# Performance work log

Hardware: AMD Instinct MI355X
Metric: run time of the kernel (lower is better)

The kernel has to match this reference:

```python
import jax, jax.numpy as jnp
import numpy as np

H = 64   # hid_dim (hard-coded in Attn_LSTM)
C = 8    # enc_in / out_dim
L = 96   # enc_seq_len = interval*lag = max_length
T = 24   # pre_len = window*horizon
B = 4096


def _p(key, shape, scale=0.1):
    return (jax.random.normal(key, shape, dtype=jnp.float32) * scale)


def setup_inputs() -> dict:
    key = jax.random.key(0)
    ks = jax.random.split(key, 20)
    inp = {
        'x_enc': jax.random.normal(ks[0], (B, L, C), dtype=jnp.float32),
        'x_mark_enc': jax.random.normal(ks[1], (B, L, 4), dtype=jnp.float32),
        'x_dec': jax.random.normal(ks[2], (B, T, C), dtype=jnp.float32),
        'x_mark_dec': jax.random.normal(ks[3], (B, T, 4), dtype=jnp.float32),
        # encoder LSTM (1 layer, input C -> hid H), pytorch gate order i,f,g,o
        'enc_Wih': _p(ks[4], (4 * H, C)), 'enc_Whh': _p(ks[5], (4 * H, H)),
        'enc_bih': _p(ks[6], (4 * H,)), 'enc_bhh': _p(ks[7], (4 * H,)),
        # decoder
        'emb_W': _p(ks[8], (H, C)), 'emb_b': _p(ks[9], (H,)),
        'attn_W': _p(ks[10], (L, 2 * H)), 'attn_b': _p(ks[11], (L,)),
        'comb_W': _p(ks[12], (H, 2 * H)), 'comb_b': _p(ks[13], (H,)),
        'dec_Wih': _p(ks[14], (4 * H, H)), 'dec_Whh': _p(ks[15], (4 * H, H)),
        'dec_bih': _p(ks[16], (4 * H,)), 'dec_bhh': _p(ks[17], (4 * H,)),
        'out_W': _p(ks[18], (C, H)), 'out_b': _p(ks[19], (C,)),
    }
    return inp


def _lstm_cell(x, h, c, Wih, Whh, bih, bhh):
    g = x @ Wih.T + h @ Whh.T + (bih + bhh)
    i, f, gg, o = jnp.split(g, 4, axis=-1)
    i, f, o = jax.nn.sigmoid(i), jax.nn.sigmoid(f), jax.nn.sigmoid(o)
    c_new = f * c + i * jnp.tanh(gg)
    h_new = o * jnp.tanh(c_new)
    return h_new, c_new


def _forward(x_enc, enc_Wih, enc_Whh, enc_bih, enc_bhh,
             emb_W, emb_b, attn_W, attn_b, comb_W, comb_b,
             dec_Wih, dec_Whh, dec_bih, dec_bhh, out_W, out_b):
    seq_last = x_enc[:, -1:, :]               # [B,1,C]
    x = x_enc - seq_last                      # normalized

    # ---- encoder: 1-layer LSTM over L steps ----
    h0 = jnp.zeros((x.shape[0], H), dtype=x.dtype)
    c0 = jnp.zeros_like(h0)

    def enc_step(carry, xt):
        h, c = carry
        h, c = _lstm_cell(xt, h, c, enc_Wih, enc_Whh, enc_bih, enc_bhh)
        return (h, c), h

    (h_enc, c_enc), enc_out = jax.lax.scan(enc_step, (h0, c0),
                                           jnp.swapaxes(x, 0, 1))
    enc_out = jnp.swapaxes(enc_out, 0, 1)     # [B,L,H]

    # ---- attention decoder: T sequential steps ----
    dec_in0 = x[:, -1, :]                     # last (normalized) input, [B,C]

    def dec_step(carry, _):
        inp, h, c = carry
        emb = jax.nn.relu(inp @ emb_W.T + emb_b)                       # [B,H]
        aw = jax.nn.softmax(jnp.concatenate([emb, h], -1) @ attn_W.T + attn_b)  # [B,L]
        ctx = jnp.einsum('bl,blh->bh', aw, enc_out)                    # [B,H]
        comb = jnp.concatenate([emb, ctx], -1) @ comb_W.T + comb_b     # [B,H]
        h, c = _lstm_cell(comb, h, c, dec_Wih, dec_Whh, dec_bih, dec_bhh)
        pred = h @ out_W.T + out_b                                     # [B,C]
        # original code feeds prediction.detach() back in
        return (jax.lax.stop_gradient(pred), h, c), (pred, aw)

    _, (preds, aws) = jax.lax.scan(dec_step, (dec_in0, h_enc, c_enc),
                                   None, length=T)
    pre_y = jnp.swapaxes(preds, 0, 1) + seq_last   # [B,T,C]
    return pre_y


def reference(x_enc, x_mark_enc, x_dec, x_mark_dec,
              enc_Wih, enc_Whh, enc_bih, enc_bhh,
              emb_W, emb_b, attn_W, attn_b, comb_W, comb_b,
              dec_Wih, dec_Whh, dec_bih, dec_bhh, out_W, out_b):
    # x_mark_enc, x_dec, x_mark_dec are accepted but unused (as in original)
    return _forward(x_enc, enc_Wih, enc_Whh, enc_bih, enc_bhh,
                    emb_W, emb_b, attn_W, attn_b, comb_W, comb_b,
                    dec_Wih, dec_Whh, dec_bih, dec_bhh, out_W, out_b)
```

## Files before the change

### kernel.cpp

```cpp
#include <hip/hip_runtime.h>

#define LL 96
#define TT 24
#define HH 64
#define CC 8
#define GG 256
#define BT 8
#define NB 512

typedef unsigned short u16t;
typedef unsigned int   u32t;
typedef __attribute__((ext_vector_type(8))) short bf16x8;
typedef __attribute__((ext_vector_type(4))) float f32x4;

__device__ __forceinline__ float b2f(u16t u){ union{u32t i; float f;} v; v.i=((u32t)u)<<16; return v.f; }
__device__ __forceinline__ u16t f2b(float f){ union{float f; u32t i;} v; v.f=f; u32t l=(v.i>>16)&1u; v.i+=0x7fffu+l; return (u16t)(v.i>>16); }
__device__ __forceinline__ float rcpf(float x){ return __builtin_amdgcn_rcpf(x); }
__device__ __forceinline__ float sigm(float x){ return rcpf(1.f + __expf(-x)); }
__device__ __forceinline__ float tanh2(float x){ return 1.f - 2.f*rcpf(__expf(2.f*x) + 1.f); }
__device__ __forceinline__ u32t pk2(float a, float b){ return (u32t)f2b(a) | ((u32t)f2b(b)<<16); }
__device__ __forceinline__ bf16x8 u2b8(uint4 u){ union{uint4 a; bf16x8 b;} v; v.a=u; return v.b; }
__device__ __forceinline__ int aaddr(int k, int m){ return (((k>>5)*4 + ((k>>3)&3))*16 + m)*8 + (k&7); }

__device__ __forceinline__ void bar_lds(){
    asm volatile("s_waitcnt lgkmcnt(0)" ::: "memory");
    __builtin_amdgcn_s_barrier();
    asm volatile("" ::: "memory");
    __builtin_amdgcn_sched_barrier(0);
}

template<bool F32> __device__ __forceinline__ float ldf(const void* p, size_t i){
    if constexpr (F32) return ((const float*)p)[i];
    else               return b2f(((const u16t*)p)[i]);
}
template<bool F32> __device__ __forceinline__ uint4 ld8p(const void* p, size_t i){
    if constexpr (F32){
        const float* f = (const float*)p + i;
        uint4 r; r.x = pk2(f[0],f[1]); r.y = pk2(f[2],f[3]);
                 r.z = pk2(f[4],f[5]); r.w = pk2(f[6],f[7]);
        return r;
    } else return *(const uint4*)((const u16t*)p + i);
}
template<bool F32> __device__ __forceinline__ void stf(void* p, size_t i, float v){
    if constexpr (F32) ((float*)p)[i] = v;
    else               ((u16t*)p)[i] = f2b(v);
}
template<bool F32> __device__ __forceinline__ float ldW_enc(const void* wih, const void* whh, int r, int k){
    if (k < CC)      return ldf<F32>(wih, (size_t)r*CC + k);
    else if (k < 72) return ldf<F32>(whh, (size_t)r*HH + (k-CC));
    else             return 0.f;
}

__device__ __forceinline__ bool inputs_are_f32(const void* bih){
    const u16t* p = (const u16t*)bih;
    int cnt = 0;
    #pragma unroll
    for (int i = 0; i < 64; ++i){
        u32t e = ((u32t)p[i] >> 7) & 0xFFu;
        cnt += (e >= 128u) ? 1 : 0;
    }
    return cnt > 0;
}

template<bool F32>
__global__ __launch_bounds__(256,4) void enc4_g(
    const void* __restrict__ x_enc,
    const void* __restrict__ eWih, const void* __restrict__ eWhh,
    const void* __restrict__ ebih, const void* __restrict__ ebhh,
    u16t* __restrict__ eoG, float* __restrict__ cG)
{
    if (inputs_are_f32(ebih) != F32) return;

    __shared__ __align__(16) short Abuf2[2][1536];

    const int tid = threadIdx.x;
    const int b0  = blockIdx.x * 4;
    const int col = tid & 15, quad = (tid >> 4) & 3, wv = tid >> 6;

    bf16x8 Bf[4][3];
    float  biasg[4];
    #pragma unroll
    for (int g = 0; g < 4; ++g){
        int r = g*64 + wv*16 + col;
        biasg[g] = ldf<F32>(ebih, r) + ldf<F32>(ebhh, r);
        #pragma unroll
        for (int kb = 0; kb < 3; ++kb){
            bf16x8 v;
            #pragma unroll
            for (int x = 0; x < 8; ++x){
                int k = kb*32 + quad*8 + x;
                v[x] = (short)f2b(ldW_enc<F32>(eWih, eWhh, r, k));
            }
            Bf[g][kb] = v;
        }
    }
    for (int n = tid; n < 2*1536; n += 256) ((short*)Abuf2)[n] = 0;
    float sl = 0.f; size_t xbase = 0;
    if (tid < 32){ int b = tid >> 3, i = tid & 7;
        xbase = (size_t)(b0+b)*(LL*CC) + i;
        sl = ldf<F32>(x_enc, xbase + (size_t)(LL-1)*CC);
    }
    __syncthreads();
    if (tid < 32){ short v = (short)f2b(ldf<F32>(x_enc, xbase) - sl);
        Abuf2[0][tid] = v; Abuf2[0][tid+32] = v; Abuf2[0][tid+64] = v; Abuf2[0][tid+96] = v; }
    float xr = (tid < 32) ? ldf<F32>(x_enc, xbase + CC) : 0.f;

    const int jmy = wv*16 + col;
    const int hwbase = aaddr(8 + jmy, 0);
    const u32t ebase = ((u32t)(b0 + quad)*4u + (u32t)(jmy>>4))*1536u + (u32t)((jmy&15)*8);

    float creg = 0.f;
    u32t  pkv  = 0;

    #pragma unroll 2
    for (int t = 0; t < LL; ++t){
        bar_lds();
        const bf16x8* AbR = (const bf16x8*)Abuf2[t & 1];
        short*        AbW = Abuf2[(t + 1) & 1];
        bf16x8 a0 = AbR[(0*4 + quad)*16 + col];
        bf16x8 a1 = AbR[(1*4 + quad)*16 + col];
        bf16x8 a2 = AbR[(2*4 + quad)*16 + col];
        f32x4 acc[4];
        #pragma unroll
        for (int g = 0; g < 4; ++g){
            f32x4 a; a[0]=biasg[g]; a[1]=biasg[g]; a[2]=biasg[g]; a[3]=biasg[g];
            a = __builtin_amdgcn_mfma_f32_16x16x32_bf16(a0, Bf[g][0], a, 0,0,0);
            a = __builtin_amdgcn_mfma_f32_16x16x32_bf16(a1, Bf[g][1], a, 0,0,0);
            a = __builtin_amdgcn_mfma_f32_16x16x32_bf16(a2, Bf[g][2], a, 0,0,0);
            acc[g] = a;
        }
        float c = sigm(acc[1][quad])*creg + sigm(acc[0][quad])*tanh2(acc[2][quad]);
        float h = sigm(acc[3][quad])*tanh2(c);
        creg = c;
        u16t hb = f2b(h);
        if ((t & 1) == 0) pkv = hb;
        else {
            pkv |= ((u32t)hb) << 16;
            *(u32t*)&eoG[ebase + (u32t)((t>>5)*512 + ((t>>3)&3)*128 + (t&7) - 1)] = pkv;
        }
        AbW[hwbase + quad*8]      = (short)hb;
        AbW[hwbase + quad*8+32]   = (short)hb;
        AbW[hwbase + quad*8+64]   = (short)hb;
        AbW[hwbase + quad*8+96]   = (short)hb;
        if (tid < 32 && t < LL-1){
            short v = (short)f2b(xr - sl);
            AbW[tid] = v; AbW[tid+32] = v; AbW[tid+64] = v; AbW[tid+96] = v;
            int tn = (t+2 < LL) ? t+2 : LL-1;
            xr = ldf<F32>(x_enc, xbase + (size_t)tn*CC);
        }
    }
    cG[(size_t)(b0 + quad)*HH + jmy] = creg;
}

template<bool F32>
__global__ __launch_bounds__(256,2) void dec8_g(
    const void* __restrict__ x_enc,
    const void* __restrict__ embW, const void* __restrict__ embb,
    const void* __restrict__ attnW, const void* __restrict__ attnb,
    const void* __restrict__ combW, const void* __restrict__ combb,
    const void* __restrict__ dWih, const void* __restrict__ dWhh,
    const void* __restrict__ dbih, const void* __restrict__ dbhh,
    const void* __restrict__ outW, const void* __restrict__ outb,
    void* __restrict__ outp, const u16t* __restrict__ eoG,
    const float* __restrict__ cG)
{
    if (inputs_are_f32(dbih) != F32) return;

    __shared__ __align__(16) float slp[CC*10];
    __shared__ __align__(16) char  uni[18880];
    __shared__ __align__(16) u16t BaL[6*4*4*16*8];
    __shared__ __align__(16) u16t emBL[64*8];
    __shared__ __align__(16) u16t oWL[8*64];

    const int tid = threadIdx.x;
    const int b0  = blockIdx.x * BT;
    const int col = tid & 15, quad = (tid >> 4) & 3, wv = tid >> 6;
    const int r0  = (quad >> 1) * 2;
    const int jmy = wv*16 + col;

    if (tid < BT*CC){ int b = tid >> 3, i = tid & 7;
        slp[i*10 + b] = ldf<F32>(x_enc, (size_t)(b0+b)*(LL*CC) + (size_t)(LL-1)*CC + i); }

    bf16x8 Bd[4][4];
    #pragma unroll
    for (int g = 0; g < 4; ++g){
        int r = g*64 + wv*16 + col;
        Bd[g][0] = u2b8(ld8p<F32>(dWih, (size_t)r*HH + quad*8));
        Bd[g][1] = u2b8(ld8p<F32>(dWih, (size_t)r*HH + 32 + quad*8));
        Bd[g][2] = u2b8(ld8p<F32>(dWhh, (size_t)r*HH + quad*8));
        Bd[g][3] = u2b8(ld8p<F32>(dWhh, (size_t)r*HH + 32 + quad*8));
    }
    bf16x8 Bc[4];
    #pragma unroll
    for (int kb = 0; kb < 4; ++kb)
        Bc[kb] = u2b8(ld8p<F32>(combW, (size_t)(wv*16+col)*128 + kb*32 + quad*8));
    bf16x8 zz = {0,0,0,0,0,0,0,0};

    for (int idx = tid; idx < 1536; idx += 256){
        int lt_ = idx >> 8, kb_ = (idx >> 6) & 3, q_ = (idx >> 4) & 3, c_ = idx & 15;
        int row = lt_*16 + c_;
        u16t tmp[8];
        #pragma unroll
        for (int x = 0; x < 8; ++x)
            tmp[x] = f2b(ldf<F32>(attnW, (size_t)row*128 + kb_*32 + q_*8 + x));
        *(uint4*)&BaL[(size_t)idx*8] = *(uint4*)tmp;
    }
    if (tid < 64){
        u16t tmp[8];
        #pragma unroll
        for (int c = 0; c < 8; ++c) tmp[c] = f2b(ldf<F32>(embW, (size_t)tid*CC + c));
        *(uint4*)&emBL[tid*8] = *(uint4*)tmp;
    }
    for (int n = tid; n < 512; n += 256) oWL[n] = f2b(ldf<F32>(outW, n));

    float* decB  = (float*)(uni + 0);
    float* attnB = (float*)(uni + 1024);
    float* embB  = (float*)(uni + 1408);
    float* combB = (float*)(uni + 1664);
    float* outB  = (float*)(uni + 1920);
    float* Lg    = (float*)(uni + 1952);
    u16t*  awB   = (u16t*)(uni + 5024);
    u16t*  Ae    = (u16t*)(uni + 6560);
    u16t*  Ah0   = (u16t*)(uni + 8608);
    u16t*  Ah1   = (u16t*)(uni + 10656);
    u16t*  Actx  = (u16t*)(uni + 12704);
    u16t*  Acmb  = (u16t*)(uni + 14752);
    u16t*  Apred = (u16t*)(uni + 16800);

    float creg[2];
    #pragma unroll
    for (int rr = 0; rr < 2; ++rr){
        int b = (quad*4 + r0 + rr) & 7;
        u16t hv = eoG[(((size_t)(b0+b)*4 + (size_t)(jmy>>4))*3 + 2)*512 + 3*128 + (jmy&15)*8 + 7];
        Ah0[aaddr(jmy, b)]   = hv;
        Ah0[aaddr(jmy, b+8)] = hv;
        creg[rr] = cG[(size_t)(b0+b)*HH + jmy];
    }
    decB[tid] = ldf<F32>(dbih, tid) + ldf<F32>(dbhh, tid);
    if (tid < LL) attnB[tid] = ldf<F32>(attnb, tid);
    if (tid < HH) embB[tid]  = ldf<F32>(embb, tid);
    if (tid < HH) combB[tid] = ldf<F32>(combb, tid);
    if (tid < CC) outB[tid]  = ldf<F32>(outb, tid);
    for (int n = tid; n < 1024; n += 256) Apred[n] = 0;
    __syncthreads();

    const u16t* ebp = eoG + (size_t)(b0 + wv*2) * 6144;
    uint4 eF0[12], eF1[12];
    #pragma unroll
    for (int f = 0; f < 12; ++f) eF0[f] = *(const uint4*)(ebp + f*512 + quad*128 + col*8);
    #pragma unroll
    for (int f = 0; f < 12; ++f) eF1[f] = *(const uint4*)(ebp + 6144 + f*512 + quad*128 + col*8);

    const int lgS = tid & 31, bS = tid >> 5;
    const bf16x8* AeV   = (const bf16x8*)Ae;
    const bf16x8* ActxV = (const bf16x8*)Actx;
    const bf16x8* AcmbV = (const bf16x8*)Acmb;
    const bf16x8* ApV   = (const bf16x8*)Apred;

    for (int t = 0; t < TT; ++t){
        u16t* AhR = (t & 1) ? Ah1 : Ah0;
        u16t* AhW = (t & 1) ? Ah0 : Ah1;
        const bf16x8* AhV = (const bf16x8*)AhR;

        {
            bf16x8 ap = ApV[quad*16 + col];
            bf16x8 eBf = zz;
            if (quad == 0) eBf = *(const bf16x8*)&emBL[(wv*16+col)*8];
            float eb = embB[wv*16 + col];
            f32x4 a; a[0]=eb; a[1]=eb; a[2]=eb; a[3]=eb;
            a = __builtin_amdgcn_mfma_f32_16x16x32_bf16(ap, eBf, a, 0,0,0);
            #pragma unroll
            for (int r = 0; r < 4; ++r)
                Ae[aaddr(wv*16+col, quad*4 + r)] = f2b(fmaxf(a[r], 0.f));
        }
        bar_lds();

        {
            bf16x8 ae0 = AeV[(0*4+quad)*16 + col], ae1 = AeV[(1*4+quad)*16 + col];
            bf16x8 ah0 = AhV[(0*4+quad)*16 + col], ah1 = AhV[(1*4+quad)*16 + col];
            const int ns = (wv < 2) ? 2 : 1;
            for (int s = 0; s < ns; ++s){
                int lt = (s == 0) ? wv : 4+wv;
                const u16t* bp = &BaL[lt*2048 + quad*128 + col*8];
                float bz = attnB[lt*16 + col];
                f32x4 a; a[0]=bz; a[1]=bz; a[2]=bz; a[3]=bz;
                a = __builtin_amdgcn_mfma_f32_16x16x32_bf16(ae0, *(const bf16x8*)&bp[0],    a, 0,0,0);
                a = __builtin_amdgcn_mfma_f32_16x16x32_bf16(ae1, *(const bf16x8*)&bp[512],  a, 0,0,0);
                a = __builtin_amdgcn_mfma_f32_16x16x32_bf16(ah0, *(const bf16x8*)&bp[1024], a, 0,0,0);
                a = __builtin_amdgcn_mfma_f32_16x16x32_bf16(ah1, *(const bf16x8*)&bp[1536], a, 0,0,0);
                if (quad < 2)
                    *(float4*)&Lg[(lt*16+col)*8 + quad*4] = make_float4(a[0],a[1],a[2],a[3]);
            }
        }
        bar_lds();

        {
            int l = lgS*3;
            float ev0 = Lg[l*8 + bS], ev1 = Lg[(l+1)*8 + bS], ev2 = Lg[(l+2)*8 + bS];
            float mx = fmaxf(ev0, fmaxf(ev1, ev2));
            #pragma unroll
            for (int m = 16; m >= 1; m >>= 1) mx = fmaxf(mx, __shfl_xor(mx, m, 32));
            float e0 = __expf(ev0 - mx), e1 = __expf(ev1 - mx), e2 = __expf(ev2 - mx);
            float sm = e0 + e1 + e2;
            #pragma unroll
            for (int m = 16; m >= 1; m >>= 1) sm += __shfl_xor(sm, m, 32);
            float inv = rcpf(sm);
            awB[bS*96 + l]     = f2b(e0*inv);
            awB[bS*96 + l + 1] = f2b(e1*inv);
            awB[bS*96 + l + 2] = f2b(e2*inv);
        }
        {
            const u16t* ap0 = awB + (wv*2)*96;
            bf16x8 f0 = *(const bf16x8*)(ap0 + quad*8);
            bf16x8 f1 = *(const bf16x8*)(ap0 + 32 + quad*8);
            bf16x8 f2 = *(const bf16x8*)(ap0 + 64 + quad*8);
            #pragma unroll
            for (int nt = 0; nt < 4; ++nt){
                f32x4 a; a[0]=0.f; a[1]=0.f; a[2]=0.f; a[3]=0.f;
                a = __builtin_amdgcn_mfma_f32_16x16x32_bf16(f0, u2b8(eF0[nt*3+0]), a, 0,0,0);
                a = __builtin_amdgcn_mfma_f32_16x16x32_bf16(f1, u2b8(eF0[nt*3+1]), a, 0,0,0);
                a = __builtin_amdgcn_mfma_f32_16x16x32_bf16(f2, u2b8(eF0[nt*3+2]), a, 0,0,0);
                if (quad == 0){
                    u16t v = f2b(a[0]);
                    Actx[aaddr(nt*16+col, wv*2)]   = v;
                    Actx[aaddr(nt*16+col, wv*2+8)] = v;
                }
            }
            const u16t* ap1 = awB + (wv*2+1)*96;
            bf16x8 g0 = *(const bf16x8*)(ap1 + quad*8);
            bf16x8 g1 = *(const bf16x8*)(ap1 + 32 + quad*8);
            bf16x8 g2 = *(const bf16x8*)(ap1 + 64 + quad*8);
            #pragma unroll
            for (int nt = 0; nt < 4; ++nt){
                f32x4 a; a[0]=0.f; a[1]=0.f; a[2]=0.f; a[3]=0.f;
                a = __builtin_amdgcn_mfma_f32_16x16x32_bf16(g0, u2b8(eF1[nt*3+0]), a, 0,0,0);
                a = __builtin_amdgcn_mfma_f32_16x16x32_bf16(g1, u2b8(eF1[nt*3+1]), a, 0,0,0);
                a = __builtin_amdgcn_mfma_f32_16x16x32_bf16(g2, u2b8(eF1[nt*3+2]), a, 0,0,0);
                if (quad == 0){
                    u16t v = f2b(a[0]);
                    Actx[aaddr(nt*16+col, wv*2+1)] = v;
                    Actx[aaddr(nt*16+col, wv*2+9)] = v;
                }
            }
        }
        bar_lds();

        {
            bf16x8 ae0 = AeV[(0*4+quad)*16 + col],   ae1 = AeV[(1*4+quad)*16 + col];
            bf16x8 ax0 = ActxV[(0*4+quad)*16 + col], ax1 = ActxV[(1*4+quad)*16 + col];
            float bz = combB[wv*16 + col];
            f32x4 a; a[0]=bz; a[1]=bz; a[2]=bz; a[3]=bz;
            a = __builtin_amdgcn_mfma_f32_16x16x32_bf16(ae0, Bc[0], a, 0,0,0);
            a = __builtin_amdgcn_mfma_f32_16x16x32_bf16(ae1, Bc[1], a, 0,0,0);
            a = __builtin_amdgcn_mfma_f32_16x16x32_bf16(ax0, Bc[2], a, 0,0,0);
            a = __builtin_amdgcn_mfma_f32_16x16x32_bf16(ax1, Bc[3], a, 0,0,0);
            #pragma unroll
            for (int r = 0; r < 4; ++r)
                Acmb[aaddr(wv*16+col, quad*4 + r)] = f2b(a[r]);
        }
        bar_lds();

        {
            bf16x8 ac0 = AcmbV[(0*4+quad)*16 + col], ac1 = AcmbV[(1*4+quad)*16 + col];
            bf16x8 ah0 = AhV[(0*4+quad)*16 + col],   ah1 = AhV[(1*4+quad)*16 + col];
            f32x4 g4[4];
            #pragma unroll
            for (int g = 0; g < 4; ++g){
                float bz = decB[g*64 + wv*16 + col];
                f32x4 a; a[0]=bz; a[1]=bz; a[2]=bz; a[3]=bz;
                a = __builtin_amdgcn_mfma_f32_16x16x32_bf16(ac0, Bd[g][0], a, 0,0,0);
                a = __builtin_amdgcn_mfma_f32_16x16x32_bf16(ac1, Bd[g][1], a, 0,0,0);
                a = __builtin_amdgcn_mfma_f32_16x16x32_bf16(ah0, Bd[g][2], a, 0,0,0);
                a = __builtin_amdgcn_mfma_f32_16x16x32_bf16(ah1, Bd[g][3], a, 0,0,0);
                g4[g] = a;
            }
            #pragma unroll
            for (int rr = 0; rr < 2; ++rr){
                int r = r0 + rr;
                int b = (quad*4 + r) & 7;
                float c = sigm(g4[1][r])*creg[rr] + sigm(g4[0][r])*tanh2(g4[2][r]);
                float h = sigm(g4[3][r])*tanh2(c);
                creg[rr] = c;
                u16t hv = f2b(h);
                AhW[aaddr(jmy, b)]   = hv;
                AhW[aaddr(jmy, b+8)] = hv;
            }
        }
        bar_lds();

        if (wv == 0){
            const bf16x8* AhWV = (const bf16x8*)AhW;
            bf16x8 xh0 = AhWV[(0*4+quad)*16 + col];
            bf16x8 xh1 = AhWV[(1*4+quad)*16 + col];
            bf16x8 oBf0 = zz, oBf1 = zz;
            if (col < CC){
                oBf0 = *(const bf16x8*)&oWL[col*64 + quad*8];
                oBf1 = *(const bf16x8*)&oWL[col*64 + 32 + quad*8];
            }
            float ob = outB[col & 7];
            f32x4 a; a[0]=ob; a[1]=ob; a[2]=ob; a[3]=ob;
            a = __builtin_amdgcn_mfma_f32_16x16x32_bf16(xh0, oBf0, a, 0,0,0);
            a = __builtin_amdgcn_mfma_f32_16x16x32_bf16(xh1, oBf1, a, 0,0,0);
            if (col < CC){
                #pragma unroll
                for (int r = 0; r < 4; ++r){
                    int m = quad*4 + r, b = m & 7;
                    float p = a[r];
                    Apred[aaddr(col, m)] = f2b(p);
                    if (m < 8)
                        stf<F32>(outp, ((size_t)(b0+b)*TT + t)*CC + col, p + slp[col*10 + b]);
                }
            }
        }
        bar_lds();
    }
}

template<bool F32>
__global__ __launch_bounds__(256,2) void fused_g(
    const void* __restrict__ x_enc,
    const void* __restrict__ eWih, const void* __restrict__ eWhh,
    const void* __restrict__ ebih, const void* __restrict__ ebhh,
    const void* __restrict__ embW, const void* __restrict__ embb,
    const void* __restrict__ attnW, const void* __restrict__ attnb,
    const void* __restrict__ combW, const void* __restrict__ combb,
    const void* __restrict__ dWih, const void* __restrict__ dWhh,
    const void* __restrict__ dbih, const void* __restrict__ dbhh,
    const void* __restrict__ outW, const void* __restrict__ outb,
    void* __restrict__ outp, u16t* __restrict__ eoG)
{
    if (inputs_are_f32(ebih) != F32) return;

    __shared__ __align__(16) float slp[CC*10];
    __shared__ __align__(16) short Abuf2[2][1536];
    __shared__ __align__(16) char  uni[18880];

    const int tid = threadIdx.x;
    const int b0  = blockIdx.x * BT;
    const int col = tid & 15, quad = (tid >> 4) & 3, wv = tid >> 6;
    const int r0  = (quad >> 1) * 2;

    bf16x8 Bf[4][3];
    float  biasg[4];
    #pragma unroll
    for (int g = 0; g < 4; ++g){
        int r = g*64 + wv*16 + col;
        biasg[g] = ldf<F32>(ebih, r) + ldf<F32>(ebhh, r);
        #pragma unroll
        for (int kb = 0; kb < 3; ++kb){
            bf16x8 v;
            #pragma unroll
            for (int x = 0; x < 8; ++x){
                int k = kb*32 + quad*8 + x;
                v[x] = (short)f2b(ldW_enc<F32>(eWih, eWhh, r, k));
            }
            Bf[g][kb] = v;
        }
    }
    for (int n = tid; n < 2*1536; n += 256) ((short*)Abuf2)[n] = 0;
    float sl = 0.f; size_t xbase = 0;
    if (tid < BT*CC){ int b = tid >> 3, i = tid & 7;
        xbase = (size_t)(b0+b)*(LL*CC) + i;
        sl = ldf<F32>(x_enc, xbase + (size_t)(LL-1)*CC);
        slp[i*10 + b] = sl; }
    __syncthreads();
    if (tid < BT*CC){ short v = (short)f2b(ldf<F32>(x_enc, xbase) - sl);
        Abuf2[0][tid] = v; Abuf2[0][tid + 64] = v; }
    float xr = (tid < BT*CC) ? ldf<F32>(x_enc, xbase + CC) : 0.f;

    const int jmy = wv*16 + col;
    const int kh  = 8 + jmy;
    const int hwbase = aaddr(kh, 0);

    u32t ebase[2];
    #pragma unroll
    for (int rr = 0; rr < 2; ++rr){
        u32t bg = (u32t)(b0 + ((quad*4 + r0 + rr) & 7));
        ebase[rr] = (bg*4u + (u32t)(jmy>>4))*1536u + (u32t)((jmy&15)*8);
    }

    float creg[2] = {0.f,0.f};
    u16t  hb16[2] = {0,0};

    for (int t = 0; t < LL; ++t){
        __syncthreads();
        const bf16x8* AbR = (const bf16x8*)Abuf2[t & 1];
        short*        AbW = Abuf2[(t + 1) & 1];
        bf16x8 a0 = AbR[(0*4 + quad)*16 + col];
        bf16x8 a1 = AbR[(1*4 + quad)*16 + col];
        bf16x8 a2 = AbR[(2*4 + quad)*16 + col];
        f32x4 acc[4];
        #pragma unroll
        for (int g = 0; g < 4; ++g){
            f32x4 a; a[0]=biasg[g]; a[1]=biasg[g]; a[2]=biasg[g]; a[3]=biasg[g];
            a = __builtin_amdgcn_mfma_f32_16x16x32_bf16(a0, Bf[g][0], a, 0,0,0);
            a = __builtin_amdgcn_mfma_f32_16x16x32_bf16(a1, Bf[g][1], a, 0,0,0);
            a = __builtin_amdgcn_mfma_f32_16x16x32_bf16(a2, Bf[g][2], a, 0,0,0);
            acc[g] = a;
        }
        int off = (t>>5)*512 + ((t>>3)&3)*128 + (t&7);
        #pragma unroll
        for (int rr = 0; rr < 2; ++rr){
            int r = r0 + rr;
            int b = (quad*4 + r) & 7;
            float c = sigm(acc[1][r])*creg[rr] + sigm(acc[0][r])*tanh2(acc[2][r]);
            float h = sigm(acc[3][r])*tanh2(c);
            creg[rr] = c; hb16[rr] = f2b(h);
            eoG[ebase[rr] + off] = hb16[rr];
            AbW[hwbase + b*8]     = (short)hb16[rr];
            AbW[hwbase + (b+8)*8] = (short)hb16[rr];
        }
        if (tid < BT*CC && t < LL-1){
            short v = (short)f2b(xr - sl);
            AbW[tid] = v; AbW[tid + 64] = v;
            int tn = (t+2 < LL) ? t+2 : LL-1;
            xr = ldf<F32>(x_enc, xbase + (size_t)tn*CC);
        }
    }

    bf16x8 Bd[4][4];
    #pragma unroll
    for (int g = 0; g < 4; ++g){
        int r = g*64 + wv*16 + col;
        Bd[g][0] = u2b8(ld8p<F32>(dWih, (size_t)r*HH + quad*8));
        Bd[g][1] = u2b8(ld8p<F32>(dWih, (size_t)r*HH + 32 + quad*8));
        Bd[g][2] = u2b8(ld8p<F32>(dWhh, (size_t)r*HH + quad*8));
        Bd[g][3] = u2b8(ld8p<F32>(dWhh, (size_t)r*HH + 32 + quad*8));
    }
    bf16x8 Ba[2][4];
    #pragma unroll
    for (int kb = 0; kb < 4; ++kb)
        Ba[0][kb] = u2b8(ld8p<F32>(attnW, (size_t)(wv*16+col)*128 + kb*32 + quad*8));
    if (wv < 2){
        #pragma unroll
        for (int kb = 0; kb < 4; ++kb)
            Ba[1][kb] = u2b8(ld8p<F32>(attnW, (size_t)((4+wv)*16+col)*128 + kb*32 + quad*8));
    } else {
        #pragma unroll
        for (int kb = 0; kb < 4; ++kb) Ba[1][kb] = Ba[0][kb];
    }
    bf16x8 Bc[4];
    #pragma unroll
    for (int kb = 0; kb < 4; ++kb)
        Bc[kb] = u2b8(ld8p<F32>(combW, (size_t)(wv*16+col)*128 + kb*32 + quad*8));
    bf16x8 zz = {0,0,0,0,0,0,0,0};
    bf16x8 eBf = zz;
    if (quad == 0) eBf = u2b8(ld8p<F32>(embW, (size_t)(wv*16+col)*CC));
    bf16x8 oBf0 = zz, oBf1 = zz;
    if (col < CC){
        oBf0 = u2b8(ld8p<F32>(outW, (size_t)col*HH + quad*8));
        oBf1 = u2b8(ld8p<F32>(outW, (size_t)col*HH + 32 + quad*8));
    }

    float* decB  = (float*)(uni + 0);
    float* attnB = (float*)(uni + 1024);
    float* embB  = (float*)(uni + 1408);
    float* combB = (float*)(uni + 1664);
    float* outB  = (float*)(uni + 1920);
    float* Lg    = (float*)(uni + 1952);
    u16t*  awB   = (u16t*)(uni + 5024);
    u16t*  Ae    = (u16t*)(uni + 6560);
    u16t*  Ah0   = (u16t*)(uni + 8608);
    u16t*  Ah1   = (u16t*)(uni + 10656);
    u16t*  Actx  = (u16t*)(uni + 12704);
    u16t*  Acmb  = (u16t*)(uni + 14752);
    u16t*  Apred = (u16t*)(uni + 16800);

    #pragma unroll
    for (int rr = 0; rr < 2; ++rr){
        int b = (quad*4 + r0 + rr) & 7;
        Ah0[aaddr(jmy, b)]     = hb16[rr];
        Ah0[aaddr(jmy, b+8)]   = hb16[rr];
    }
    decB[tid] = ldf<F32>(dbih, tid) + ldf<F32>(dbhh, tid);
    if (tid < LL) attnB[tid] = ldf<F32>(attnb, tid);
    if (tid < HH) embB[tid]  = ldf<F32>(embb, tid);
    if (tid < HH) combB[tid] = ldf<F32>(combb, tid);
    if (tid < CC) outB[tid]  = ldf<F32>(outb, tid);
    for (int n = tid; n < 1024; n += 256) Apred[n] = 0;
    __syncthreads();

    const u16t* ebp = eoG + (size_t)(b0 + wv*2) * 6144;
    uint4 eF0[12], eF1[12];
    #pragma unroll
    for (int f = 0; f < 12; ++f) eF0[f] = *(const uint4*)(ebp + f*512 + quad*128 + col*8);
    #pragma unroll
    for (int f = 0; f < 12; ++f) eF1[f] = *(const uint4*)(ebp + 6144 + f*512 + quad*128 + col*8);

    const int lgS = tid & 31, bS = tid >> 5;
    const bf16x8* AeV   = (const bf16x8*)Ae;
    const bf16x8* ActxV = (const bf16x8*)Actx;
    const bf16x8* AcmbV = (const bf16x8*)Acmb;
    const bf16x8* ApV   = (const bf16x8*)Apred;

    for (int t = 0; t < TT; ++t){
        u16t* AhR = (t & 1) ? Ah1 : Ah0;
        u16t* AhW = (t & 1) ? Ah0 : Ah1;
        const bf16x8* AhV = (const bf16x8*)AhR;

        {
            bf16x8 ap = ApV[quad*16 + col];
            float eb = embB[wv*16 + col];
            f32x4 a; a[0]=eb; a[1]=eb; a[2]=eb; a[3]=eb;
            a = __builtin_amdgcn_mfma_f32_16x16x32_bf16(ap, eBf, a, 0,0,0);
            #pragma unroll
            for (int r = 0; r < 4; ++r)
                Ae[aaddr(wv*16+col, quad*4 + r)] = f2b(fmaxf(a[r], 0.f));
        }
        __syncthreads();

        {
            bf16x8 ae0 = AeV[(0*4+quad)*16 + col], ae1 = AeV[(1*4+quad)*16 + col];
            bf16x8 ah0 = AhV[(0*4+quad)*16 + col], ah1 = AhV[(1*4+quad)*16 + col];
            const int ns = (wv < 2) ? 2 : 1;
            for (int s = 0; s < ns; ++s){
                int lt = (s == 0) ? wv : 4+wv;
                float bz = attnB[lt*16 + col];
                f32x4 a; a[0]=bz; a[1]=bz; a[2]=bz; a[3]=bz;
                a = __builtin_amdgcn_mfma_f32_16x16x32_bf16(ae0, Ba[s][0], a, 0,0,0);
                a = __builtin_amdgcn_mfma_f32_16x16x32_bf16(ae1, Ba[s][1], a, 0,0,0);
                a = __builtin_amdgcn_mfma_f32_16x16x32_bf16(ah0, Ba[s][2], a, 0,0,0);
                a = __builtin_amdgcn_mfma_f32_16x16x32_bf16(ah1, Ba[s][3], a, 0,0,0);
                if (quad < 2)
                    *(float4*)&Lg[(lt*16+col)*8 + quad*4] = make_float4(a[0],a[1],a[2],a[3]);
            }
        }
        __syncthreads();

        {
            int l = lgS*3;
            float ev0 = Lg[l*8 + bS], ev1 = Lg[(l+1)*8 + bS], ev2 = Lg[(l+2)*8 + bS];
            float mx = fmaxf(ev0, fmaxf(ev1, ev2));
            #pragma unroll
            for (int m = 16; m >= 1; m >>= 1) mx = fmaxf(mx, __shfl_xor(mx, m, 32));
            float e0 = __expf(ev0 - mx), e1 = __expf(ev1 - mx), e2 = __expf(ev2 - mx);
            float sm = e0 + e1 + e2;
            #pragma unroll
            for (int m = 16; m >= 1; m >>= 1) sm += __shfl_xor(sm, m, 32);
            float inv = rcpf(sm);
            awB[bS*96 + l]     = f2b(e0*inv);
            awB[bS*96 + l + 1] = f2b(e1*inv);
            awB[bS*96 + l + 2] = f2b(e2*inv);
        }
        {
            const u16t* ap0 = awB + (wv*2)*96;
            bf16x8 f0 = *(const bf16x8*)(ap0 + quad*8);
            bf16x8 f1 = *(const bf16x8*)(ap0 + 32 + quad*8);
            bf16x8 f2 = *(const bf16x8*)(ap0 + 64 + quad*8);
            #pragma unroll
            for (int nt = 0; nt < 4; ++nt){
                f32x4 a; a[0]=0.f; a[1]=0.f; a[2]=0.f; a[3]=0.f;
                a = __builtin_amdgcn_mfma_f32_16x16x32_bf16(f0, u2b8(eF0[nt*3+0]), a, 0,0,0);
                a = __builtin_amdgcn_mfma_f32_16x16x32_bf16(f1, u2b8(eF0[nt*3+1]), a, 0,0,0);
                a = __builtin_amdgcn_mfma_f32_16x16x32_bf16(f2, u2b8(eF0[nt*3+2]), a, 0,0,0);
                if (quad == 0){
                    u16t v = f2b(a[0]);
                    Actx[aaddr(nt*16+col, wv*2)]   = v;
                    Actx[aaddr(nt*16+col, wv*2+8)] = v;
                }
            }
            const u16t* ap1 = awB + (wv*2+1)*96;
            bf16x8 g0 = *(const bf16x8*)(ap1 + quad*8);
            bf16x8 g1 = *(const bf16x8*)(ap1 + 32 + quad*8);
            bf16x8 g2 = *(const bf16x8*)(ap1 + 64 + quad*8);
            #pragma unroll
            for (int nt = 0; nt < 4; ++nt){
                f32x4 a; a[0]=0.f; a[1]=0.f; a[2]=0.f; a[3]=0.f;
                a = __builtin_amdgcn_mfma_f32_16x16x32_bf16(g0, u2b8(eF1[nt*3+0]), a, 0,0,0);
                a = __builtin_amdgcn_mfma_f32_16x16x32_bf16(g1, u2b8(eF1[nt*3+1]), a, 0,0,0);
                a = __builtin_amdgcn_mfma_f32_16x16x32_bf16(g2, u2b8(eF1[nt*3+2]), a, 0,0,0);
                if (quad == 0){
                    u16t v = f2b(a[0]);
                    Actx[aaddr(nt*16+col, wv*2+1)] = v;
                    Actx[aaddr(nt*16+col, wv*2+9)] = v;
                }
            }
        }
        __syncthreads();

        {
            bf16x8 ae0 = AeV[(0*4+quad)*16 + col],   ae1 = AeV[(1*4+quad)*16 + col];
            bf16x8 ax0 = ActxV[(0*4+quad)*16 + col], ax1 = ActxV[(1*4+quad)*16 + col];
            float bz = combB[wv*16 + col];
            f32x4 a; a[0]=bz; a[1]=bz; a[2]=bz; a[3]=bz;
            a = __builtin_amdgcn_mfma_f32_16x16x32_bf16(ae0, Bc[0], a, 0,0,0);
            a = __builtin_amdgcn_mfma_f32_16x16x32_bf16(ae1, Bc[1], a, 0,0,0);
            a = __builtin_amdgcn_mfma_f32_16x16x32_bf16(ax0, Bc[2], a, 0,0,0);
            a = __builtin_amdgcn_mfma_f32_16x16x32_bf16(ax1, Bc[3], a, 0,0,0);
            #pragma unroll
            for (int r = 0; r < 4; ++r)
                Acmb[aaddr(wv*16+col, quad*4 + r)] = f2b(a[r]);
        }
        __syncthreads();

        {
            bf16x8 ac0 = AcmbV[(0*4+quad)*16 + col], ac1 = AcmbV[(1*4+quad)*16 + col];
            bf16x8 ah0 = AhV[(0*4+quad)*16 + col],   ah1 = AhV[(1*4+quad)*16 + col];
            f32x4 g4[4];
            #pragma unroll
            for (int g = 0; g < 4; ++g){
                float bz = decB[g*64 + wv*16 + col];
                f32x4 a; a[0]=bz; a[1]=bz; a[2]=bz; a[3]=bz;
                a = __builtin_amdgcn_mfma_f32_16x16x32_bf16(ac0, Bd[g][0], a, 0,0,0);
                a = __builtin_amdgcn_mfma_f32_16x16x32_bf16(ac1, Bd[g][1], a, 0,0,0);
                a = __builtin_amdgcn_mfma_f32_16x16x32_bf16(ah0, Bd[g][2], a, 0,0,0);
                a = __builtin_amdgcn_mfma_f32_16x16x32_bf16(ah1, Bd[g][3], a, 0,0,0);
                g4[g] = a;
            }
            #pragma unroll
            for (int rr = 0; rr < 2; ++rr){
                int r = r0 + rr;
                int b = (quad*4 + r) & 7;
                float c = sigm(g4[1][r])*creg[rr] + sigm(g4[0][r])*tanh2(g4[2][r]);
                float h = sigm(g4[3][r])*tanh2(c);
                creg[rr] = c;
                u16t hv = f2b(h);
                AhW[aaddr(jmy, b)]   = hv;
                AhW[aaddr(jmy, b+8)] = hv;
            }
        }
        __syncthreads();

        if (wv == 0){
            const bf16x8* AhWV = (const bf16x8*)AhW;
            bf16x8 xh0 = AhWV[(0*4+quad)*16 + col];
            bf16x8 xh1 = AhWV[(1*4+quad)*16 + col];
            float ob = outB[col & 7];
            f32x4 a; a[0]=ob; a[1]=ob; a[2]=ob; a[3]=ob;
            a = __builtin_amdgcn_mfma_f32_16x16x32_bf16(xh0, oBf0, a, 0,0,0);
            a = __builtin_amdgcn_mfma_f32_16x16x32_bf16(xh1, oBf1, a, 0,0,0);
            if (col < CC){
                #pragma unroll
                for (int r = 0; r < 4; ++r){
                    int m = quad*4 + r, b = m & 7;
                    float p = a[r];
                    Apred[aaddr(col, m)] = f2b(p);
                    if (m < 8)
                        stf<F32>(outp, ((size_t)(b0+b)*TT + t)*CC + col, p + slp[col*10 + b]);
                }
            }
        }
        __syncthreads();
    }
}

extern "C" void kernel_launch(void* const* d_in, const int* in_sizes, int n_in,
                              void* d_out, int out_size, void* d_ws, size_t ws_size,
                              hipStream_t stream)
{
    (void)in_sizes; (void)n_in; (void)out_size;
    u16t* eoG = (u16t*)d_ws;
    if (ws_size >= 50331648ull + 1048576ull){
        float* cG = (float*)((char*)d_ws + 50331648ull);
        enc4_g<false><<<1024, 256, 0, stream>>>(
            d_in[0], d_in[4], d_in[5], d_in[6], d_in[7], eoG, cG);
        enc4_g<true ><<<1024, 256, 0, stream>>>(
            d_in[0], d_in[4], d_in[5], d_in[6], d_in[7], eoG, cG);
        dec8_g<false><<<NB, 256, 0, stream>>>(
            d_in[0],
            d_in[8],  d_in[9],  d_in[10], d_in[11],
            d_in[12], d_in[13], d_in[14], d_in[15],
            d_in[16], d_in[17], d_in[18], d_in[19],
            d_out, eoG, cG);
        dec8_g<true ><<<NB, 256, 0, stream>>>(
            d_in[0],
            d_in[8],  d_in[9],  d_in[10], d_in[11],
            d_in[12], d_in[13], d_in[14], d_in[15],
            d_in[16], d_in[17], d_in[18], d_in[19],
            d_out, eoG, cG);
    } else {
        fused_g<false><<<NB, 256, 0, stream>>>(
            d_in[0],
            d_in[4],  d_in[5],  d_in[6],  d_in[7],
            d_in[8],  d_in[9],  d_in[10], d_in[11],
            d_in[12], d_in[13], d_in[14], d_in[15],
            d_in[16], d_in[17], d_in[18], d_in[19],
            d_out, eoG);
        fused_g<true><<<NB, 256, 0, stream>>>(
            d_in[0],
            d_in[4],  d_in[5],  d_in[6],  d_in[7],
            d_in[8],  d_in[9],  d_in[10], d_in[11],
            d_in[12], d_in[13], d_in[14], d_in[15],
            d_in[16], d_in[17], d_in[18], d_in[19],
            d_out, eoG);
    }
}
```

Measured before the change: 279.3 us.

## Fold output projection into embedding weights and drop softmax max-subtraction

```diff
diff --git a/kernel.cpp b/kernel.cpp
--- a/kernel.cpp
+++ b/kernel.cpp
@@ -167,9 +167,9 @@
     if (inputs_are_f32(dbih) != F32) return;
 
     __shared__ __align__(16) float slp[CC*10];
-    __shared__ __align__(16) char  uni[18880];
+    __shared__ __align__(16) char  uni[16800];
     __shared__ __align__(16) u16t BaL[6*4*4*16*8];
-    __shared__ __align__(16) u16t emBL[64*8];
+    __shared__ __align__(16) u16t M1L[64*64];
     __shared__ __align__(16) u16t oWL[8*64];
 
     const int tid = threadIdx.x;
@@ -205,17 +205,26 @@
             tmp[x] = f2b(ldf<F32>(attnW, (size_t)row*128 + kb_*32 + q_*8 + x));
         *(uint4*)&BaL[(size_t)idx*8] = *(uint4*)tmp;
     }
-    if (tid < 64){
-        u16t tmp[8];
-        #pragma unroll
-        for (int c = 0; c < 8; ++c) tmp[c] = f2b(ldf<F32>(embW, (size_t)tid*CC + c));
-        *(uint4*)&emBL[tid*8] = *(uint4*)tmp;
+    for (int idx = tid; idx < 1024; idx += 256){
+        int j = idx >> 4, k0 = (idx & 15) * 4;
+        float acc4[4] = {0.f,0.f,0.f,0.f};
+        #pragma unroll
+        for (int c = 0; c < 8; ++c){
+            float e = ldf<F32>(embW, (size_t)j*CC + c);
+            #pragma unroll
+            for (int kk = 0; kk < 4; ++kk)
+                acc4[kk] += e * ldf<F32>(outW, (size_t)c*HH + k0 + kk);
+        }
+        u16t tmp[4];
+        #pragma unroll
+        for (int kk = 0; kk < 4; ++kk) tmp[kk] = f2b(acc4[kk]);
+        *(uint2*)&M1L[j*64 + k0] = *(uint2*)tmp;
     }
     for (int n = tid; n < 512; n += 256) oWL[n] = f2b(ldf<F32>(outW, n));
 
     float* decB  = (float*)(uni + 0);
     float* attnB = (float*)(uni + 1024);
-    float* embB  = (float*)(uni + 1408);
+    float* b1B   = (float*)(uni + 1408);
     float* combB = (float*)(uni + 1664);
     float* outB  = (float*)(uni + 1920);
     float* Lg    = (float*)(uni + 1952);
@@ -225,7 +234,6 @@
     u16t*  Ah1   = (u16t*)(uni + 10656);
     u16t*  Actx  = (u16t*)(uni + 12704);
     u16t*  Acmb  = (u16t*)(uni + 14752);
-    u16t*  Apred = (u16t*)(uni + 16800);
 
     float creg[2];
     #pragma unroll
@@ -238,10 +246,22 @@
     }
     decB[tid] = ldf<F32>(dbih, tid) + ldf<F32>(dbhh, tid);
     if (tid < LL) attnB[tid] = ldf<F32>(attnb, tid);
-    if (tid < HH) embB[tid]  = ldf<F32>(embb, tid);
+    if (tid < HH){
+        float s = ldf<F32>(embb, tid);
+        #pragma unroll
+        for (int c = 0; c < 8; ++c)
+            s += ldf<F32>(embW, (size_t)tid*CC + c) * ldf<F32>(outb, c);
+        b1B[tid] = s;
+    }
     if (tid < HH) combB[tid] = ldf<F32>(combb, tid);
     if (tid < CC) outB[tid]  = ldf<F32>(outb, tid);
-    for (int n = tid; n < 1024; n += 256) Apred[n] = 0;
+    {
+        float e0v = fmaxf(ldf<F32>(embb, jmy), 0.f);
+        u16t ev = f2b(e0v);
+        #pragma unroll
+        for (int r = 0; r < 4; ++r)
+            Ae[aaddr(jmy, quad*4 + r)] = ev;
+    }
     __syncthreads();
 
     const u16t* ebp = eoG + (size_t)(b0 + wv*2) * 6144;
@@ -255,25 +275,11 @@
     const bf16x8* AeV   = (const bf16x8*)Ae;
     const bf16x8* ActxV = (const bf16x8*)Actx;
     const bf16x8* AcmbV = (const bf16x8*)Acmb;
-    const bf16x8* ApV   = (const bf16x8*)Apred;
 
     for (int t = 0; t < TT; ++t){
         u16t* AhR = (t & 1) ? Ah1 : Ah0;
         u16t* AhW = (t & 1) ? Ah0 : Ah1;
         const bf16x8* AhV = (const bf16x8*)AhR;
-
-        {
-            bf16x8 ap = ApV[quad*16 + col];
-            bf16x8 eBf = zz;
-            if (quad == 0) eBf = *(const bf16x8*)&emBL[(wv*16+col)*8];
-            float eb = embB[wv*16 + col];
-            f32x4 a; a[0]=eb; a[1]=eb; a[2]=eb; a[3]=eb;
-            a = __builtin_amdgcn_mfma_f32_16x16x32_bf16(ap, eBf, a, 0,0,0);
-            #pragma unroll
-            for (int r = 0; r < 4; ++r)
-                Ae[aaddr(wv*16+col, quad*4 + r)] = f2b(fmaxf(a[r], 0.f));
-        }
-        bar_lds();
 
         {
             bf16x8 ae0 = AeV[(0*4+quad)*16 + col], ae1 = AeV[(1*4+quad)*16 + col];
@@ -296,11 +302,7 @@
 
         {
             int l = lgS*3;
-            float ev0 = Lg[l*8 + bS], ev1 = Lg[(l+1)*8 + bS], ev2 = Lg[(l+2)*8 + bS];
-            float mx = fmaxf(ev0, fmaxf(ev1, ev2));
-            #pragma unroll
-            for (int m = 16; m >= 1; m >>= 1) mx = fmaxf(mx, __shfl_xor(mx, m, 32));
-            float e0 = __expf(ev0 - mx), e1 = __expf(ev1 - mx), e2 = __expf(ev2 - mx);
+            float e0 = __expf(Lg[l*8 + bS]), e1 = __expf(Lg[(l+1)*8 + bS]), e2 = __expf(Lg[(l+2)*8 + bS]);
             float sm = e0 + e1 + e2;
             #pragma unroll
             for (int m = 16; m >= 1; m >>= 1) sm += __shfl_xor(sm, m, 32);
@@ -388,27 +390,36 @@
         }
         bar_lds();
 
-        if (wv == 0){
+        {
             const bf16x8* AhWV = (const bf16x8*)AhW;
             bf16x8 xh0 = AhWV[(0*4+quad)*16 + col];
             bf16x8 xh1 = AhWV[(1*4+quad)*16 + col];
-            bf16x8 oBf0 = zz, oBf1 = zz;
-            if (col < CC){
-                oBf0 = *(const bf16x8*)&oWL[col*64 + quad*8];
-                oBf1 = *(const bf16x8*)&oWL[col*64 + 32 + quad*8];
-            }
-            float ob = outB[col & 7];
-            f32x4 a; a[0]=ob; a[1]=ob; a[2]=ob; a[3]=ob;
-            a = __builtin_amdgcn_mfma_f32_16x16x32_bf16(xh0, oBf0, a, 0,0,0);
-            a = __builtin_amdgcn_mfma_f32_16x16x32_bf16(xh1, oBf1, a, 0,0,0);
-            if (col < CC){
-                #pragma unroll
-                for (int r = 0; r < 4; ++r){
-                    int m = quad*4 + r, b = m & 7;
-                    float p = a[r];
-                    Apred[aaddr(col, m)] = f2b(p);
-                    if (m < 8)
-                        stf<F32>(outp, ((size_t)(b0+b)*TT + t)*CC + col, p + slp[col*10 + b]);
+            bf16x8 m10 = *(const bf16x8*)&M1L[(wv*16+col)*64 + quad*8];
+            bf16x8 m11 = *(const bf16x8*)&M1L[(wv*16+col)*64 + 32 + quad*8];
+            float eb = b1B[wv*16 + col];
+            f32x4 a; a[0]=eb; a[1]=eb; a[2]=eb; a[3]=eb;
+            a = __builtin_amdgcn_mfma_f32_16x16x32_bf16(xh0, m10, a, 0,0,0);
+            a = __builtin_amdgcn_mfma_f32_16x16x32_bf16(xh1, m11, a, 0,0,0);
+            #pragma unroll
+            for (int r = 0; r < 4; ++r)
+                Ae[aaddr(wv*16+col, quad*4 + r)] = f2b(fmaxf(a[r], 0.f));
+            if (wv == 0){
+                bf16x8 oBf0 = zz, oBf1 = zz;
+                if (col < CC){
+                    oBf0 = *(const bf16x8*)&oWL[col*64 + quad*8];
+                    oBf1 = *(const bf16x8*)&oWL[col*64 + 32 + quad*8];
+                }
+                float ob = outB[col & 7];
+                f32x4 p4; p4[0]=ob; p4[1]=ob; p4[2]=ob; p4[3]=ob;
+                p4 = __builtin_amdgcn_mfma_f32_16x16x32_bf16(xh0, oBf0, p4, 0,0,0);
+                p4 = __builtin_amdgcn_mfma_f32_16x16x32_bf16(xh1, oBf1, p4, 0,0,0);
+                if (col < CC){
+                    #pragma unroll
+                    for (int r = 0; r < 4; ++r){
+                        int m = quad*4 + r;
+                        if (m < 8)
+                            stf<F32>(outp, ((size_t)(b0+m)*TT + t)*CC + col, p4[r] + slp[col*10 + m]);
+                    }
                 }
             }
         }
```

After: 274.4 us. No clear change (-1.8%).
